# Optimization experiments

Measured on AMD Instinct MI355X. Metric: run time of the kernel, lower is better.

## Reference

```python
import jax, jax.numpy as jnp
import numpy as np


def _rx(theta):
    # RX(theta) = [[cos(t/2), -i sin(t/2)], [-i sin(t/2), cos(t/2)]]
    t = theta.astype(jnp.float32) if hasattr(theta, 'astype') else jnp.float32(theta)
    c = jnp.cos(t / 2).astype(jnp.complex64)
    s = (-1j) * jnp.sin(t / 2).astype(jnp.complex64)
    return jnp.stack([jnp.stack([c, s], -1), jnp.stack([s, c], -1)], -2)  # [..., 2, 2]


def _apply_1q(state, U, q):
    # state: [B, 2, 2, ..., 2] (n qubit axes after batch); gate on qubit q
    state = jnp.moveaxis(state, q + 1, -1)
    if U.ndim == 3:  # batched gate (angle embedding): U[b] applied to state[b]
        state = jnp.einsum('b...y,bxy->b...x', state, U)
    else:  # shared gate (trainable layer weights)
        state = jnp.einsum('...y,xy->...x', state, U)
    return jnp.moveaxis(state, -1, q + 1)


def _cnot(state, c, t):
    # flip target qubit t where control qubit c is |1>
    state = jnppermute = jnp.moveaxis(state, (c + 1, t + 1), (-2, -1))
    s0 = state[..., 0, :]
    s1 = state[..., 1, ::-1]
    state = jnp.stack([s0, s1], axis=-2)
    return jnp.moveaxis(state, (-2, -1), (c + 1, t + 1))


def _qpred(inputs, weights):
    B, n = inputs.shape
    L = weights.shape[0]
    # |0...0> state, shape [B] + [2]*n (qubit 0 = most-significant axis)
    state = jnp.zeros((B,) + (2,) * n, jnp.complex64)
    state = state.at[(slice(None),) + (0,) * n].set(1.0 + 0.0j)
    # AngleEmbedding: RX(inputs[:, j]) on qubit j (per-sample angle -> batched gate)
    for j in range(n):
        state = _apply_1q(state, _rx(inputs[:, j]), j)
    # BasicEntanglerLayers: RX(weights[i, j]) then CNOT ring
    for i in range(L):
        for j in range(n):
            state = _apply_1q(state, _rx(weights[i, j]), j)
        if n == 2:
            state = _cnot(state, 0, 1)
        elif n > 2:
            for j in range(n):
                state = _cnot(state, j, (j + 1) % n)
    # <Z_i> = sum_k |psi_k|^2 * (1 - 2*bit_i(k))
    probs = jnp.abs(state.reshape(B, -1)) ** 2  # [B, 2^n]
    k = np.arange(2 ** n)
    signs = (1.0 - 2.0 * ((k[None, :] >> (n - 1 - np.arange(n)[:, None])) & 1)).astype(np.float32)  # [n, 2^n]
    return probs @ jnp.asarray(signs).T  # [B, n]


def setup_inputs() -> dict:
    key = jax.random.key(0)
    k1, k2 = jax.random.split(key)
    B, n_qubits, n_qlayers = 8192, 10, 2
    inputs = jax.random.normal(k1, (B, n_qubits), dtype=jnp.float32)
    weights = jax.random.normal(k2, (n_qlayers, n_qubits), dtype=jnp.float32)
    return {"inputs": inputs, "weights": weights}


def reference(inputs, weights):
    # call(): reshape to [-1, n_qubits], run circuit, reshape back (no-op here: already 2D)
    return _qpred(inputs, weights)
```

## Files before the change

### kernel.cpp

```cpp
#include <hip/hip_runtime.h>


#define NQ 10

struct QTerms { unsigned t[1024]; int n; };

constexpr unsigned long long kLUT = 0x32DC6789AB45FE10ull;
constexpr unsigned kSIGN = 0x0480u;
constexpr int kS[NQ] = {0x1FF,0x300,0x380,0x3C0,0x3E0,0x3F0,0x3F8,0x3FC,0x3FE,0x3FF};

constexpr QTerms gen(int q) {
    QTerms r{};
    const int s = kS[q];
    int pc = 0;
    for (int c = 0; c < NQ; ++c) pc += (s >> c) & 1;
    const int nsub = 1 << pc;
    for (int i = 0; i < nsub; ++i) {
        unsigned code = 0, tmask = 0;
        int rem = i;
        for (int c = 0; c < NQ; ++c) {
            if ((s >> c) & 1) {
                if (rem & 1) { code |= 2u << (2*c); tmask |= 1u << c; }
                else         { code |= 3u << (2*c); }
                rem >>= 1;
            }
        }
        unsigned sign = 0;
        for (int st = 0; st < NQ; ++st) {
            const int cc = st, tt = (st + 9) % NQ;
            const unsigned p_c = (code >> (2*cc)) & 3u;
            const unsigned p_t = (code >> (2*tt)) & 3u;
            const unsigned idx = (p_c << 2) | p_t;
            const unsigned nib = (unsigned)((kLUT >> (4*idx)) & 0xFull);
            code &= ~((3u << (2*cc)) | (3u << (2*tt)));
            code |= (nib >> 2) << (2*cc);
            code |= (nib & 3u) << (2*tt);
            sign ^= (kSIGN >> idx) & 1u;
        }
        unsigned zm = 0, ym = 0; bool dead = false;
        for (int c = 0; c < NQ; ++c) {
            const unsigned p = (code >> (2*c)) & 3u;
            if (p == 1u) dead = true;
            else if (p == 3u) zm |= 1u << c;
            else if (p == 2u) ym |= 1u << c;
        }
        if (dead) continue;
        r.t[r.n++] = tmask | (zm << 10) | (ym << 20) | (sign << 30);
    }
    return r;
}

constexpr QTerms cT0 = gen(0); constexpr QTerms cT1 = gen(1);
constexpr QTerms cT2 = gen(2); constexpr QTerms cT3 = gen(3);
constexpr QTerms cT4 = gen(4); constexpr QTerms cT5 = gen(5);
constexpr QTerms cT6 = gen(6); constexpr QTerms cT7 = gen(7);
constexpr QTerms cT8 = gen(8); constexpr QTerms cT9 = gen(9);

__device__ const QTerms dT0 = cT0; __device__ const QTerms dT1 = cT1;
__device__ const QTerms dT2 = cT2; __device__ const QTerms dT3 = cT3;
__device__ const QTerms dT4 = cT4; __device__ const QTerms dT5 = cT5;
__device__ const QTerms dT6 = cT6; __device__ const QTerms dT7 = cT7;
__device__ const QTerms dT8 = cT8; __device__ const QTerms dT9 = cT9;

constexpr int kN[NQ] = {cT0.n, cT1.n, cT2.n, cT3.n, cT4.n,
                        cT5.n, cT6.n, cT7.n, cT8.n, cT9.n};

template<int LMASK>
__device__ __forceinline__ float lxor(float x, int a32) {
    if constexpr (LMASK == 1)
        return __int_as_float(__builtin_amdgcn_update_dpp(
            __float_as_int(x), __float_as_int(x), 0xB1, 0xF, 0xF, true));
    else if constexpr (LMASK == 2)
        return __int_as_float(__builtin_amdgcn_update_dpp(
            __float_as_int(x), __float_as_int(x), 0x4E, 0xF, 0xF, true));
    else if constexpr (LMASK == 8)
        return __int_as_float(__builtin_amdgcn_update_dpp(
            __float_as_int(x), __float_as_int(x), 0x128, 0xF, 0xF, true));
    else if constexpr (LMASK == 32)
        return __int_as_float(__builtin_amdgcn_ds_bpermute(a32, __float_as_int(x)));
    else
        return __int_as_float(__builtin_amdgcn_ds_swizzle(
            __float_as_int(x), (LMASK << 10) | 0x1F));
}

template<int Q>
__device__ __forceinline__ float eval_q(const unsigned* __restrict__ tq,
                                        const float (&g)[NQ], const float (&sg)[NQ],
                                        const float (&cz)[NQ], const float (&sy)[NQ],
                                        int lane) {
    constexpr int S = kS[Q];
    constexpr int N = kN[Q];
    float ssum = 0.f;
    for (int t = lane; t < N; t += 64) {
        const unsigned w = tq[t];
        float p = 1.f;
        #pragma unroll
        for (int c = 0; c < NQ; ++c) {
            if ((S >> c) & 1)
                p *= ((w >> c) & 1u) ? sg[c] : g[c];
            const unsigned zb = (w >> (10 + c)) & 1u;
            const unsigned yb = (w >> (20 + c)) & 1u;
            float f = zb ? cz[c] : 1.f;
            f = yb ? sy[c] : f;
            p *= f;
        }
        ssum += (w & (1u << 30)) ? -p : p;
    }
    return ssum;
}

__global__ __launch_bounds__(256)
void eval_kernel(const float* __restrict__ inputs,
                 const float* __restrict__ weights,
                 float* __restrict__ out, int B)
{
    const int wave = (blockIdx.x * blockDim.x + threadIdx.x) >> 6;
    const int lane = threadIdx.x & 63;
    if (wave >= B) return;
    const int a32 = (lane ^ 32) << 2;

    float g[NQ], sg[NQ], cz[NQ], sy[NQ];
    const float* xe = inputs + wave * NQ;
    #pragma unroll
    for (int c = 0; c < NQ; ++c) {
        const float th = weights[NQ + 9 - c];
        __sincosf(th, &sg[c], &g[c]);
        const float a = xe[9 - c] + weights[9 - c];
        float sn, cs; __sincosf(a, &sn, &cs);
        cz[c] = cs; sy[c] = -sn;
    }

    float res[NQ];
    res[0] = eval_q<0>(dT0.t, g, sg, cz, sy, lane);
    res[1] = eval_q<1>(dT1.t, g, sg, cz, sy, lane);
    res[2] = eval_q<2>(dT2.t, g, sg, cz, sy, lane);
    res[3] = eval_q<3>(dT3.t, g, sg, cz, sy, lane);
    res[4] = eval_q<4>(dT4.t, g, sg, cz, sy, lane);
    res[5] = eval_q<5>(dT5.t, g, sg, cz, sy, lane);
    res[6] = eval_q<6>(dT6.t, g, sg, cz, sy, lane);
    res[7] = eval_q<7>(dT7.t, g, sg, cz, sy, lane);
    res[8] = eval_q<8>(dT8.t, g, sg, cz, sy, lane);
    res[9] = eval_q<9>(dT9.t, g, sg, cz, sy, lane);

    #pragma unroll
    for (int q = 0; q < NQ; ++q) res[q] += lxor< 1>(res[q], a32);
    #pragma unroll
    for (int q = 0; q < NQ; ++q) res[q] += lxor< 2>(res[q], a32);
    #pragma unroll
    for (int q = 0; q < NQ; ++q) res[q] += lxor< 8>(res[q], a32);
    #pragma unroll
    for (int q = 0; q < NQ; ++q) res[q] += lxor< 4>(res[q], a32);
    #pragma unroll
    for (int q = 0; q < NQ; ++q) res[q] += lxor<16>(res[q], a32);
    #pragma unroll
    for (int q = 0; q < NQ; ++q) res[q] += lxor<32>(res[q], a32);

    float v = 0.f;
    #pragma unroll
    for (int q = 0; q < NQ; ++q)
        if (lane == q) v = res[q];
    if (lane < NQ) out[wave * NQ + lane] = v;
}

extern "C" void kernel_launch(void* const* d_in, const int* in_sizes, int n_in,
                              void* d_out, int out_size, void* d_ws, size_t ws_size,
                              hipStream_t stream) {
    const float* inputs  = (const float*)d_in[0];
    const float* weights = (const float*)d_in[1];
    float* out = (float*)d_out;
    const int B = in_sizes[0] / NQ;
    eval_kernel<<<(B + 3) / 4, 256, 0, stream>>>(inputs, weights, out, B);
}
```

Measured before the change: 67.61 us.

## Precompute batch-independent weight coefficients in a separate kernel

Adds a small pre-kernel that, for every term of every qubit, folds the sign and the product of second-layer weight sin/cos factors into one float coefficient, written to the workspace alongside the term mask. The main kernel then starts each term product from that coefficient and only multiplies by the per-sample input factors, skipping qubit positions that never carry a Z or Y bit (compile-time mask). This removes per-sample recomputation of the weight-only factors and cuts the multiply chain, at the cost of an extra launch and 8-byte loads instead of 4-byte loads per term.

```diff
diff --git a/kernel.cpp b/kernel.cpp
--- a/kernel.cpp
+++ b/kernel.cpp
@@ -56,14 +56,67 @@
 constexpr QTerms cT6 = gen(6); constexpr QTerms cT7 = gen(7);
 constexpr QTerms cT8 = gen(8); constexpr QTerms cT9 = gen(9);
 
-__device__ const QTerms dT0 = cT0; __device__ const QTerms dT1 = cT1;
-__device__ const QTerms dT2 = cT2; __device__ const QTerms dT3 = cT3;
-__device__ const QTerms dT4 = cT4; __device__ const QTerms dT5 = cT5;
-__device__ const QTerms dT6 = cT6; __device__ const QTerms dT7 = cT7;
-__device__ const QTerms dT8 = cT8; __device__ const QTerms dT9 = cT9;
-
 constexpr int kN[NQ] = {cT0.n, cT1.n, cT2.n, cT3.n, cT4.n,
                         cT5.n, cT6.n, cT7.n, cT8.n, cT9.n};
+
+struct Flat { unsigned w[4096]; unsigned cm[4096]; int off[11]; };
+
+constexpr void appendF(Flat& f, const QTerms& T, int S, int q, int& k) {
+    f.off[q] = k;
+    for (int j = 0; j < T.n; ++j) {
+        const unsigned w = T.t[j];
+        f.w[k]  = w;
+        f.cm[k] = (unsigned)S & ~(w & 0x3FFu);
+        ++k;
+    }
+}
+
+constexpr Flat buildFlat() {
+    Flat f{};
+    int k = 0;
+    appendF(f, cT0, kS[0], 0, k); appendF(f, cT1, kS[1], 1, k);
+    appendF(f, cT2, kS[2], 2, k); appendF(f, cT3, kS[3], 3, k);
+    appendF(f, cT4, kS[4], 4, k); appendF(f, cT5, kS[5], 5, k);
+    appendF(f, cT6, kS[6], 6, k); appendF(f, cT7, kS[7], 7, k);
+    appendF(f, cT8, kS[8], 8, k); appendF(f, cT9, kS[9], 9, k);
+    f.off[10] = k;
+    return f;
+}
+
+constexpr Flat cF = buildFlat();
+constexpr int kTOT = cF.off[10];
+constexpr int kOff[NQ] = {cF.off[0],cF.off[1],cF.off[2],cF.off[3],cF.off[4],
+                          cF.off[5],cF.off[6],cF.off[7],cF.off[8],cF.off[9]};
+
+constexpr unsigned calcU(int q) {
+    unsigned u = 0;
+    for (int j = cF.off[q]; j < cF.off[q+1]; ++j) {
+        const unsigned w = cF.w[j];
+        u |= ((w >> 10) & 0x3FFu) | ((w >> 20) & 0x3FFu);
+    }
+    return u;
+}
+constexpr unsigned kU[NQ] = {calcU(0),calcU(1),calcU(2),calcU(3),calcU(4),
+                             calcU(5),calcU(6),calcU(7),calcU(8),calcU(9)};
+
+__device__ const Flat dF = cF;
+
+__global__ __launch_bounds__(256)
+void coef_kernel(const float* __restrict__ weights, float2* __restrict__ coefs) {
+    const int i = blockIdx.x * blockDim.x + threadIdx.x;
+    if (i >= kTOT) return;
+    const unsigned w  = dF.w[i];
+    const unsigned cm = dF.cm[i];
+    float C = (w & (1u << 30)) ? -1.f : 1.f;
+    #pragma unroll
+    for (int c = 0; c < NQ; ++c) {
+        float sn, cs;
+        __sincosf(weights[NQ + 9 - c], &sn, &cs);
+        if ((w >> c) & 1u)       C *= sn;
+        else if ((cm >> c) & 1u) C *= cs;
+    }
+    coefs[i] = make_float2(C, __uint_as_float(w));
+}
 
 template<int LMASK>
 __device__ __forceinline__ float lxor(float x, int a32) {
@@ -84,27 +137,28 @@
 }
 
 template<int Q>
-__device__ __forceinline__ float eval_q(const unsigned* __restrict__ tq,
-                                        const float (&g)[NQ], const float (&sg)[NQ],
+__device__ __forceinline__ float eval_q(const float2* __restrict__ coefs,
                                         const float (&cz)[NQ], const float (&sy)[NQ],
                                         int lane) {
-    constexpr int S = kS[Q];
     constexpr int N = kN[Q];
+    constexpr int OFF = kOff[Q];
+    constexpr unsigned U = kU[Q];
     float ssum = 0.f;
     for (int t = lane; t < N; t += 64) {
-        const unsigned w = tq[t];
-        float p = 1.f;
+        const float2 r = coefs[OFF + t];
+        const unsigned w = __float_as_uint(r.y);
+        float p = r.x;
         #pragma unroll
         for (int c = 0; c < NQ; ++c) {
-            if ((S >> c) & 1)
-                p *= ((w >> c) & 1u) ? sg[c] : g[c];
-            const unsigned zb = (w >> (10 + c)) & 1u;
-            const unsigned yb = (w >> (20 + c)) & 1u;
-            float f = zb ? cz[c] : 1.f;
-            f = yb ? sy[c] : f;
-            p *= f;
-        }
-        ssum += (w & (1u << 30)) ? -p : p;
+            if ((U >> c) & 1u) {
+                const unsigned zb = (w >> (10 + c)) & 1u;
+                const unsigned yb = (w >> (20 + c)) & 1u;
+                float f = zb ? cz[c] : 1.f;
+                f = yb ? sy[c] : f;
+                p *= f;
+            }
+        }
+        ssum += p;
     }
     return ssum;
 }
@@ -112,6 +166,7 @@
 __global__ __launch_bounds__(256)
 void eval_kernel(const float* __restrict__ inputs,
                  const float* __restrict__ weights,
+                 const float2* __restrict__ coefs,
                  float* __restrict__ out, int B)
 {
     const int wave = (blockIdx.x * blockDim.x + threadIdx.x) >> 6;
@@ -119,28 +174,26 @@
     if (wave >= B) return;
     const int a32 = (lane ^ 32) << 2;
 
-    float g[NQ], sg[NQ], cz[NQ], sy[NQ];
+    float cz[NQ], sy[NQ];
     const float* xe = inputs + wave * NQ;
     #pragma unroll
     for (int c = 0; c < NQ; ++c) {
-        const float th = weights[NQ + 9 - c];
-        __sincosf(th, &sg[c], &g[c]);
         const float a = xe[9 - c] + weights[9 - c];
         float sn, cs; __sincosf(a, &sn, &cs);
         cz[c] = cs; sy[c] = -sn;
     }
 
     float res[NQ];
-    res[0] = eval_q<0>(dT0.t, g, sg, cz, sy, lane);
-    res[1] = eval_q<1>(dT1.t, g, sg, cz, sy, lane);
-    res[2] = eval_q<2>(dT2.t, g, sg, cz, sy, lane);
-    res[3] = eval_q<3>(dT3.t, g, sg, cz, sy, lane);
-    res[4] = eval_q<4>(dT4.t, g, sg, cz, sy, lane);
-    res[5] = eval_q<5>(dT5.t, g, sg, cz, sy, lane);
-    res[6] = eval_q<6>(dT6.t, g, sg, cz, sy, lane);
-    res[7] = eval_q<7>(dT7.t, g, sg, cz, sy, lane);
-    res[8] = eval_q<8>(dT8.t, g, sg, cz, sy, lane);
-    res[9] = eval_q<9>(dT9.t, g, sg, cz, sy, lane);
+    res[0] = eval_q<0>(coefs, cz, sy, lane);
+    res[1] = eval_q<1>(coefs, cz, sy, lane);
+    res[2] = eval_q<2>(coefs, cz, sy, lane);
+    res[3] = eval_q<3>(coefs, cz, sy, lane);
+    res[4] = eval_q<4>(coefs, cz, sy, lane);
+    res[5] = eval_q<5>(coefs, cz, sy, lane);
+    res[6] = eval_q<6>(coefs, cz, sy, lane);
+    res[7] = eval_q<7>(coefs, cz, sy, lane);
+    res[8] = eval_q<8>(coefs, cz, sy, lane);
+    res[9] = eval_q<9>(coefs, cz, sy, lane);
 
     #pragma unroll
     for (int q = 0; q < NQ; ++q) res[q] += lxor< 1>(res[q], a32);
@@ -169,5 +222,9 @@
     const float* weights = (const float*)d_in[1];
     float* out = (float*)d_out;
     const int B = in_sizes[0] / NQ;
-    eval_kernel<<<(B + 3) / 4, 256, 0, stream>>>(inputs, weights, out, B);
-}
+
+    float2* coefs = (float2*)d_ws;
+
+    coef_kernel<<<(kTOT + 255) / 256, 256, 0, stream>>>(weights, coefs);
+    eval_kernel<<<(B + 3) / 4, 256, 0, stream>>>(inputs, weights, coefs, out, B);
+}
```

After: 65.05 us. 1.04x faster.
